# Performance work log

Hardware: AMD Instinct MI355X
Metric: run time of the kernel (lower is better)

The kernel has to match this reference:

```python
import jax, jax.numpy as jnp
import numpy as np

N = 100000   # nodes
E = 1600000  # edges (avg degree 16)
IN, HID, OUT = 128, 128, 64


def _glorot(key, shape):
    limit = np.sqrt(6.0 / (shape[0] + shape[1])).astype(np.float32)
    return jax.random.uniform(key, shape, jnp.float32, -limit, limit)


def setup_inputs() -> dict:
    key = jax.random.key(0)
    ks = jax.random.split(key, 12)
    inp = {}
    for i, (f, s, d) in enumerate([("feat1", "src1", "dst1"), ("feat2", "src2", "dst2"), ("feat", "src", "dst")]):
        inp[f] = jax.random.normal(ks[3 * i], (N, IN), jnp.float32)
        inp[s] = jax.random.randint(ks[3 * i + 1], (E,), 0, N, jnp.int32)
        inp[d] = jax.random.randint(ks[3 * i + 2], (E,), 0, N, jnp.int32)
    inp["W1"] = _glorot(ks[9], (IN, HID))
    inp["b1"] = jnp.zeros((HID,), jnp.float32)
    inp["W2"] = _glorot(ks[10], (HID, OUT))
    inp["b2"] = jnp.zeros((OUT,), jnp.float32)
    return inp


def _gcn_layer(x, src, dst, W, b):
    # DGL GraphConv norm='both': D_dst^{-1/2} * A * D_src^{-1/2} * X * W + b
    ones = jnp.ones(src.shape, jnp.float32)
    deg_out = jax.ops.segment_sum(ones, src, num_segments=N)
    deg_in = jax.ops.segment_sum(ones, dst, num_segments=N)
    norm_src = jax.lax.rsqrt(jnp.maximum(deg_out, 1.0))
    norm_dst = jax.lax.rsqrt(jnp.maximum(deg_in, 1.0))
    h = (x @ W) * norm_src[:, None]           # transform then normalize (math-equivalent order)
    agg = jax.ops.segment_sum(h[src], dst, num_segments=N)  # spmm aggregate
    return agg * norm_dst[:, None] + b


def _encoder(x, src, dst, W1, b1, W2, b2):
    h = jax.nn.relu(_gcn_layer(x, src, dst, W1, b1))
    return _gcn_layer(h, src, dst, W2, b2)


def reference(feat1, src1, dst1, feat2, src2, dst2, feat, src, dst, W1, b1, W2, b2):
    z1 = _encoder(feat1, src1, dst1, W1, b1, W2, b2)
    z2 = _encoder(feat2, src2, dst2, W1, b1, W2, b2)
    z = _encoder(feat, src, dst, W1, b1, W2, b2)
    return (z1, z2, z)
```

## Files before the change

### kernel.cpp

```cpp
#include <hip/hip_runtime.h>

#define NNODES 100000
#define NEDGES 1600000
#define FIN 128
#define FHID 128
#define FOUT 64

typedef unsigned short u16;
typedef unsigned char u8;
typedef unsigned int u32;
typedef __attribute__((ext_vector_type(8))) short short8;
typedef __attribute__((ext_vector_type(4))) float floatx4;

__device__ __forceinline__ u16 f2bf(float f) {
  u32 u = __float_as_uint(f);
  u32 r = (u + 0x7fffu + ((u >> 16) & 1u)) >> 16;
  return (u16)r;
}


#define NBUK 391
#define NSL2 250
#define SLICE2 (NEDGES / NSL2)

__global__ __launch_bounds__(256) void bucket_hist_kernel(const int* __restrict__ src,
                                                          const int* __restrict__ dst,
                                                          u32* __restrict__ part,
                                                          u32* __restrict__ part_src, int E) {
  __shared__ u32 hd[NBUK], hs[NBUK];
  const int s = blockIdx.x;
  for (int i = threadIdx.x; i < NBUK; i += 256) { hd[i] = 0; hs[i] = 0; }
  __syncthreads();
  const int e0 = s * SLICE2, e1 = min(e0 + SLICE2, E);
  const int i0 = e0 >> 2, i1 = e1 >> 2;
  for (int i = i0 + threadIdx.x; i < i1; i += 256) {
    int4 dv = ((const int4*)dst)[i];
    int4 sv = ((const int4*)src)[i];
    atomicAdd(&hd[(u32)dv.x >> 8], 1u);
    atomicAdd(&hd[(u32)dv.y >> 8], 1u);
    atomicAdd(&hd[(u32)dv.z >> 8], 1u);
    atomicAdd(&hd[(u32)dv.w >> 8], 1u);
    atomicAdd(&hs[(u32)sv.x >> 8], 1u);
    atomicAdd(&hs[(u32)sv.y >> 8], 1u);
    atomicAdd(&hs[(u32)sv.z >> 8], 1u);
    atomicAdd(&hs[(u32)sv.w >> 8], 1u);
  }
  __syncthreads();
  for (int i = threadIdx.x; i < NBUK; i += 256) {
    part[(size_t)s * NBUK + i] = hd[i];
    part_src[(size_t)s * NBUK + i] = hs[i];
  }
}

__global__ __launch_bounds__(512) void scan_part_kernel(u32* __restrict__ part_d,
                                                        u32* __restrict__ boff_d,
                                                        u32* __restrict__ bcount_d,
                                                        u32* __restrict__ part_s,
                                                        u32* __restrict__ boff_s,
                                                        u32* __restrict__ bcount_s) {
  u32* __restrict__ part = blockIdx.x ? part_s : part_d;
  u32* __restrict__ boff = blockIdx.x ? boff_s : boff_d;
  u32* __restrict__ bcount = blockIdx.x ? bcount_s : bcount_d;
  const int b = threadIdx.x;
  u32 run = 0;
  if (b < NBUK) {
#pragma unroll 5
    for (int s = 0; s < NSL2; s++) {
      u32 v = part[(size_t)s * NBUK + b];
      part[(size_t)s * NBUK + b] = run;
      run += v;
    }
  }
  __shared__ u32 sh[512];
  sh[threadIdx.x] = (b < NBUK) ? run : 0;
  __syncthreads();
  for (int d = 1; d < 512; d <<= 1) {
    u32 t = (threadIdx.x >= d) ? sh[threadIdx.x - d] : 0;
    __syncthreads();
    sh[threadIdx.x] += t;
    __syncthreads();
  }
  if (b < NBUK) {
    boff[b] = sh[threadIdx.x] - run;
    bcount[b] = run;
  }
}

__global__ __launch_bounds__(256) void scatter_kernel(const int* __restrict__ src,
                                                      const int* __restrict__ dst,
                                                      const u32* __restrict__ part,
                                                      const u32* __restrict__ boff,
                                                      const u32* __restrict__ part_src,
                                                      const u32* __restrict__ boff_src,
                                                      u32* __restrict__ pe,
                                                      u8* __restrict__ pes, int E) {
  __shared__ u32 cur[NBUK], curs[NBUK];
  const int s = blockIdx.x;
  for (int i = threadIdx.x; i < NBUK; i += 256) {
    cur[i] = part[(size_t)s * NBUK + i] + boff[i];
    curs[i] = part_src[(size_t)s * NBUK + i] + boff_src[i];
  }
  __syncthreads();
  const int e0 = s * SLICE2, e1 = min(e0 + SLICE2, E);
  const int i0 = e0 >> 2, i1 = e1 >> 2;
  for (int i = i0 + threadIdx.x; i < i1; i += 256) {
    int4 sv = ((const int4*)src)[i];
    int4 dv = ((const int4*)dst)[i];
    u32 p;
    p = atomicAdd(&cur[(u32)dv.x >> 8], 1u); pe[p] = ((u32)sv.x << 8) | ((u32)dv.x & 255u);
    p = atomicAdd(&cur[(u32)dv.y >> 8], 1u); pe[p] = ((u32)sv.y << 8) | ((u32)dv.y & 255u);
    p = atomicAdd(&cur[(u32)dv.z >> 8], 1u); pe[p] = ((u32)sv.z << 8) | ((u32)dv.z & 255u);
    p = atomicAdd(&cur[(u32)dv.w >> 8], 1u); pe[p] = ((u32)sv.w << 8) | ((u32)dv.w & 255u);
    p = atomicAdd(&curs[(u32)sv.x >> 8], 1u); pes[p] = (u8)((u32)sv.x & 255u);
    p = atomicAdd(&curs[(u32)sv.y >> 8], 1u); pes[p] = (u8)((u32)sv.y & 255u);
    p = atomicAdd(&curs[(u32)sv.z >> 8], 1u); pes[p] = (u8)((u32)sv.z & 255u);
    p = atomicAdd(&curs[(u32)sv.w >> 8], 1u); pes[p] = (u8)((u32)sv.w & 255u);
  }
}

__global__ __launch_bounds__(256) void bucket_csr_kernel(const u32* __restrict__ pe,
                                                         const u32* __restrict__ boff,
                                                         const u32* __restrict__ bcount,
                                                         int* __restrict__ csr,
                                                         int* __restrict__ offs,
                                                         int* __restrict__ deg_dst,
                                                         float* __restrict__ norm_dst, int n) {
  const int b = blockIdx.x;
  const int beg = (int)boff[b];
  const int cnt = (int)bcount[b];
  __shared__ int h[256], loc[256];
  const int t = threadIdx.x;
  h[t] = 0;
  __syncthreads();
  for (int i = t; i < cnt; i += 256) atomicAdd(&h[pe[beg + i] & 255u], 1);
  __syncthreads();
  const int myc = h[t];
  loc[t] = myc;
  __syncthreads();
  for (int d = 1; d < 256; d <<= 1) {
    int v = (t >= d) ? loc[t - d] : 0;
    __syncthreads();
    loc[t] += v;
    __syncthreads();
  }
  const int start = beg + loc[t] - myc;
  const int node = b * 256 + t;
  if (node < n) {
    offs[node] = start;
    deg_dst[node] = myc;
    norm_dst[node] = rsqrtf(fmaxf((float)myc, 1.0f));
  }
  __syncthreads();
  h[t] = start;
  __syncthreads();
  for (int i = t; i < cnt; i += 256) {
    u32 v = pe[beg + i];
    int p = atomicAdd(&h[v & 255u], 1);
    csr[p] = (int)(v >> 8);
  }
}

__global__ __launch_bounds__(256) void bucket_count_src_kernel(const u8* __restrict__ pes,
                                                               const u32* __restrict__ boff,
                                                               const u32* __restrict__ bcount,
                                                               float* __restrict__ norm_src,
                                                               int n) {
  const int b = blockIdx.x;
  const int beg = (int)boff[b];
  const int cnt = (int)bcount[b];
  __shared__ int h[256];
  h[threadIdx.x] = 0;
  __syncthreads();
  for (int i = threadIdx.x; i < cnt; i += 256) atomicAdd(&h[pes[beg + i]], 1);
  __syncthreads();
  const int node = b * 256 + threadIdx.x;
  if (node < n) norm_src[node] = rsqrtf(fmaxf((float)h[threadIdx.x], 1.0f));
}


#define XP 136

template <int CTOT, bool IN_BF16>
__global__ __launch_bounds__(256) void gemm_mfma(const void* __restrict__ Xv,
                                                 const float* __restrict__ W,
                                                 const float* __restrict__ norm,
                                                 u16* __restrict__ Y, int nrows) {
  __shared__ u16 Xs[64 * XP];
  __shared__ u16 Wt[64 * XP];
  __shared__ float norm_s[64];
  const int tid = threadIdx.x;
  const int row0 = blockIdx.x * 64;
  const int col0 = blockIdx.y * 64;

  if constexpr (IN_BF16) {
    const u16* X = (const u16*)Xv;
    for (int i = tid; i < 64 * 16; i += 256) {
      int r = i >> 4, k8 = (i & 15) * 8;
      int gr = row0 + r;
      uint4 v = make_uint4(0u, 0u, 0u, 0u);
      if (gr < nrows) v = *(const uint4*)&X[(size_t)gr * 128 + k8];
      *(uint4*)&Xs[r * XP + k8] = v;
    }
  } else {
    const float* X = (const float*)Xv;
    for (int i = tid; i < 64 * 32; i += 256) {
      int r = i >> 5, k4 = (i & 31) * 4;
      int gr = row0 + r;
      ushort4 o = make_ushort4(0, 0, 0, 0);
      if (gr < nrows) {
        float4 v = *(const float4*)&X[(size_t)gr * 128 + k4];
        o.x = f2bf(v.x); o.y = f2bf(v.y); o.z = f2bf(v.z); o.w = f2bf(v.w);
      }
      *(ushort4*)&Xs[r * XP + k4] = o;
    }
  }
  for (int i = tid; i < 128 * 16; i += 256) {
    int k = i >> 4, c4 = (i & 15) * 4;
    float4 v = *(const float4*)&W[(size_t)k * CTOT + col0 + c4];
    Wt[(c4 + 0) * XP + k] = f2bf(v.x);
    Wt[(c4 + 1) * XP + k] = f2bf(v.y);
    Wt[(c4 + 2) * XP + k] = f2bf(v.z);
    Wt[(c4 + 3) * XP + k] = f2bf(v.w);
  }
  if (tid < 64) norm_s[tid] = (row0 + tid < nrows) ? norm[row0 + tid] : 0.f;
  __syncthreads();

  const int w = tid >> 6, lane = tid & 63;
  const int quad = lane >> 4, r16 = lane & 15;
  const int arow = w * 16 + r16;

  short8 a[4];
#pragma unroll
  for (int kc = 0; kc < 4; kc++)
    a[kc] = *(const short8*)&Xs[arow * XP + kc * 32 + quad * 8];

#pragma unroll
  for (int nc = 0; nc < 4; nc++) {
    floatx4 acc = {0.f, 0.f, 0.f, 0.f};
#pragma unroll
    for (int kc = 0; kc < 4; kc++) {
      short8 b = *(const short8*)&Wt[(nc * 16 + r16) * XP + kc * 32 + quad * 8];
      acc = __builtin_amdgcn_mfma_f32_16x16x32_bf16(a[kc], b, acc, 0, 0, 0);
    }
#pragma unroll
    for (int i = 0; i < 4; i++) {
      int lr = w * 16 + quad * 4 + i;
      int gr = row0 + lr;
      if (gr < nrows)
        Y[(size_t)gr * CTOT + col0 + nc * 16 + r16] = f2bf(acc[i] * norm_s[lr]);
    }
  }
}


__device__ __forceinline__ void acc_row(float* acc, uint4 p) {
  acc[0] += __uint_as_float(p.x << 16);
  acc[1] += __uint_as_float(p.x & 0xffff0000u);
  acc[2] += __uint_as_float(p.y << 16);
  acc[3] += __uint_as_float(p.y & 0xffff0000u);
  acc[4] += __uint_as_float(p.z << 16);
  acc[5] += __uint_as_float(p.z & 0xffff0000u);
  acc[6] += __uint_as_float(p.w << 16);
  acc[7] += __uint_as_float(p.w & 0xffff0000u);
}

template <int F, bool RELU, bool OUT_BF16>
__global__ __launch_bounds__(256) void spmm_bf16(const u16* __restrict__ Hb,
                                                 const int* __restrict__ offs,
                                                 const int* __restrict__ deg,
                                                 const int* __restrict__ csr,
                                                 const float* __restrict__ norm_dst,
                                                 const float* __restrict__ bias,
                                                 void* __restrict__ Yv, int n) {
  constexpr int TPN = F / 8;
  constexpr int NPB = 256 / TPN;
  int node = blockIdx.x * NPB + threadIdx.x / TPN;
  if (node >= n) return;
  int f0 = (threadIdx.x % TPN) * 8;
  int beg = offs[node];
  int end = beg + deg[node];
  const u16* __restrict__ Hp = Hb + f0;
  float acc[8] = {};
  int e = beg;
  for (; e + 4 <= end; e += 4) {
    int s0 = csr[e + 0];
    int s1 = csr[e + 1];
    int s2 = csr[e + 2];
    int s3 = csr[e + 3];
    uint4 p0 = *(const uint4*)&Hp[(size_t)s0 * F];
    uint4 p1 = *(const uint4*)&Hp[(size_t)s1 * F];
    uint4 p2 = *(const uint4*)&Hp[(size_t)s2 * F];
    uint4 p3 = *(const uint4*)&Hp[(size_t)s3 * F];
    acc_row(acc, p0);
    acc_row(acc, p1);
    acc_row(acc, p2);
    acc_row(acc, p3);
  }
  for (; e < end; e++) {
    int s = csr[e];
    uint4 p = *(const uint4*)&Hp[(size_t)s * F];
    acc_row(acc, p);
  }
  float nd = norm_dst[node];
  float o[8];
#pragma unroll
  for (int i = 0; i < 8; i++) {
    o[i] = fmaf(acc[i], nd, bias[f0 + i]);
    if (RELU) o[i] = fmaxf(o[i], 0.f);
  }
  if constexpr (OUT_BF16) {
    u16* Y = (u16*)Yv;
    uint4 pk;
    pk.x = (u32)f2bf(o[0]) | ((u32)f2bf(o[1]) << 16);
    pk.y = (u32)f2bf(o[2]) | ((u32)f2bf(o[3]) << 16);
    pk.z = (u32)f2bf(o[4]) | ((u32)f2bf(o[5]) << 16);
    pk.w = (u32)f2bf(o[6]) | ((u32)f2bf(o[7]) << 16);
    *(uint4*)&Y[(size_t)node * F + f0] = pk;
  } else {
    float* Y = (float*)Yv;
    *(float4*)&Y[(size_t)node * F + f0] = make_float4(o[0], o[1], o[2], o[3]);
    *(float4*)&Y[(size_t)node * F + f0 + 4] = make_float4(o[4], o[5], o[6], o[7]);
  }
}


extern "C" void kernel_launch(void* const* d_in, const int* in_sizes, int n_in,
                              void* d_out, int out_size, void* d_ws, size_t ws_size,
                              hipStream_t stream) {
  const int N = NNODES;
  const int E = NEDGES;
  const float* W1 = (const float*)d_in[9];
  const float* b1 = (const float*)d_in[10];
  const float* W2 = (const float*)d_in[11];
  const float* b2 = (const float*)d_in[12];

  char* ws = (char*)d_ws;
  size_t off = 0;
  auto alloc = [&](size_t bytes) -> void* {
    void* p = ws + off;
    off += (bytes + 255) & ~(size_t)255;
    return p;
  };
  int* deg_dst = (int*)alloc((size_t)N * 4);
  float* norm_src = (float*)alloc((size_t)N * 4);
  float* norm_dst = (float*)alloc((size_t)N * 4);
  int* offs = (int*)alloc((size_t)N * 4);
  u32* boff = (u32*)alloc((size_t)NBUK * 4);
  u32* bcount = (u32*)alloc((size_t)NBUK * 4);
  u32* boff_s = (u32*)alloc((size_t)NBUK * 4);
  u32* bcount_s = (u32*)alloc((size_t)NBUK * 4);
  int* csr = (int*)alloc((size_t)E * 4);
  u16* H = (u16*)alloc((size_t)N * FHID * 2);
  u16* T = (u16*)alloc((size_t)N * FHID * 2);

  u32* part = (u32*)H;
  u32* part_src = part + (size_t)NSL2 * NBUK;
  u8* pes = (u8*)(part_src + (size_t)NSL2 * NBUK);
  u32* pe = (u32*)T;

  const int gemm_rb = (N + 63) / 64;

  for (int g = 0; g < 3; g++) {
    const float* feat = (const float*)d_in[3 * g + 0];
    const int* src = (const int*)d_in[3 * g + 1];
    const int* dst = (const int*)d_in[3 * g + 2];
    float* zout = (float*)d_out + (size_t)g * N * FOUT;

    bucket_hist_kernel<<<NSL2, 256, 0, stream>>>(src, dst, part, part_src, E);
    scan_part_kernel<<<2, 512, 0, stream>>>(part, boff, bcount, part_src, boff_s, bcount_s);
    scatter_kernel<<<NSL2, 256, 0, stream>>>(src, dst, part, boff, part_src, boff_s,
                                             pe, pes, E);
    bucket_csr_kernel<<<NBUK, 256, 0, stream>>>(pe, boff, bcount, csr, offs, deg_dst,
                                                norm_dst, N);
    bucket_count_src_kernel<<<NBUK, 256, 0, stream>>>(pes, boff_s, bcount_s, norm_src, N);

    gemm_mfma<FHID, false><<<dim3(gemm_rb, FHID / 64), 256, 0, stream>>>(
        feat, W1, norm_src, H, N);
    {
      constexpr int NPB = 256 / (FHID / 8);
      spmm_bf16<FHID, true, true><<<(N + NPB - 1) / NPB, 256, 0, stream>>>(
          H, offs, deg_dst, csr, norm_dst, b1, T, N);
    }

    gemm_mfma<FOUT, true><<<dim3(gemm_rb, FOUT / 64), 256, 0, stream>>>(
        T, W2, norm_src, H, N);
    {
      constexpr int NPB = 256 / (FOUT / 8);
      spmm_bf16<FOUT, false, false><<<(N + NPB - 1) / NPB, 256, 0, stream>>>(
          H, offs, deg_dst, csr, norm_dst, b2, zout, N);
    }
  }
}
```

Measured before the change: 829.3 us.

## Batch three graph encoders into single launches via grid z dimension

All nine per-graph kernels now take a blockIdx.z graph index and per-graph workspace slices, so the three encoders run as one launch per stage instead of three sequential launches. This targets launch overhead and low occupancy in the small kernels (scan, hist, csr) by filling the GPU with three graphs' work at once. It needs three times the workspace and falls back to the per-graph loop when the workspace is too small. The spmm gather loop is also software-pipelined so the next four rows load while the current four accumulate, at some extra register cost.

```diff
diff --git a/kernel.cpp b/kernel.cpp
--- a/kernel.cpp
+++ b/kernel.cpp
@@ -12,21 +12,32 @@
 typedef __attribute__((ext_vector_type(8))) short short8;
 typedef __attribute__((ext_vector_type(4))) float floatx4;
 
+#define NBUK 391
+#define NSL2 250
+#define SLICE2 (NEDGES / NSL2)
+#define SP ((size_t)NSL2 * NBUK)
+#define NH16 ((size_t)NNODES * FHID)
+
 __device__ __forceinline__ u16 f2bf(float f) {
   u32 u = __float_as_uint(f);
   u32 r = (u + 0x7fffu + ((u >> 16) & 1u)) >> 16;
   return (u16)r;
 }
 
-
-#define NBUK 391
-#define NSL2 250
-#define SLICE2 (NEDGES / NSL2)
-
-__global__ __launch_bounds__(256) void bucket_hist_kernel(const int* __restrict__ src,
-                                                          const int* __restrict__ dst,
-                                                          u32* __restrict__ part,
-                                                          u32* __restrict__ part_src, int E) {
+__device__ __forceinline__ const int* sel(const int* a, const int* b, const int* c, int z) {
+  return z == 0 ? a : (z == 1 ? b : c);
+}
+
+
+__global__ __launch_bounds__(256) void bucket_hist_kernel(
+    const int* s0, const int* s1, const int* s2,
+    const int* d0, const int* d1, const int* d2,
+    u16* __restrict__ Hbase, int E) {
+  const int z = blockIdx.z;
+  const int* __restrict__ src = sel(s0, s1, s2, z);
+  const int* __restrict__ dst = sel(d0, d1, d2, z);
+  u32* __restrict__ part = (u32*)(Hbase + (size_t)z * NH16);
+  u32* __restrict__ part_src = part + SP;
   __shared__ u32 hd[NBUK], hs[NBUK];
   const int s = blockIdx.x;
   for (int i = threadIdx.x; i < NBUK; i += 256) { hd[i] = 0; hs[i] = 0; }
@@ -52,15 +63,16 @@
   }
 }
 
-__global__ __launch_bounds__(512) void scan_part_kernel(u32* __restrict__ part_d,
+__global__ __launch_bounds__(512) void scan_part_kernel(u16* __restrict__ Hbase,
                                                         u32* __restrict__ boff_d,
                                                         u32* __restrict__ bcount_d,
-                                                        u32* __restrict__ part_s,
                                                         u32* __restrict__ boff_s,
                                                         u32* __restrict__ bcount_s) {
-  u32* __restrict__ part = blockIdx.x ? part_s : part_d;
-  u32* __restrict__ boff = blockIdx.x ? boff_s : boff_d;
-  u32* __restrict__ bcount = blockIdx.x ? bcount_s : bcount_d;
+  const int z = blockIdx.z;
+  u32* base = (u32*)(Hbase + (size_t)z * NH16);
+  u32* __restrict__ part = blockIdx.x ? base + SP : base;
+  u32* __restrict__ boff = (blockIdx.x ? boff_s : boff_d) + (size_t)z * NBUK;
+  u32* __restrict__ bcount = (blockIdx.x ? bcount_s : bcount_d) + (size_t)z * NBUK;
   const int b = threadIdx.x;
   u32 run = 0;
   if (b < NBUK) {
@@ -86,19 +98,25 @@
   }
 }
 
-__global__ __launch_bounds__(256) void scatter_kernel(const int* __restrict__ src,
-                                                      const int* __restrict__ dst,
-                                                      const u32* __restrict__ part,
-                                                      const u32* __restrict__ boff,
-                                                      const u32* __restrict__ part_src,
-                                                      const u32* __restrict__ boff_src,
-                                                      u32* __restrict__ pe,
-                                                      u8* __restrict__ pes, int E) {
+__global__ __launch_bounds__(256) void scatter_kernel(
+    const int* s0, const int* s1, const int* s2,
+    const int* d0, const int* d1, const int* d2,
+    u16* __restrict__ Hbase, u16* __restrict__ Tbase,
+    const u32* __restrict__ boff_d, const u32* __restrict__ boff_src, int E) {
+  const int z = blockIdx.z;
+  const int* __restrict__ src = sel(s0, s1, s2, z);
+  const int* __restrict__ dst = sel(d0, d1, d2, z);
+  const u32* __restrict__ part = (const u32*)(Hbase + (size_t)z * NH16);
+  const u32* __restrict__ part_src = part + SP;
+  u8* __restrict__ pes = (u8*)(part_src + SP);
+  u32* __restrict__ pe = (u32*)(Tbase + (size_t)z * NH16);
+  const u32* __restrict__ boff = boff_d + (size_t)z * NBUK;
+  const u32* __restrict__ boff_s = boff_src + (size_t)z * NBUK;
   __shared__ u32 cur[NBUK], curs[NBUK];
   const int s = blockIdx.x;
   for (int i = threadIdx.x; i < NBUK; i += 256) {
     cur[i] = part[(size_t)s * NBUK + i] + boff[i];
-    curs[i] = part_src[(size_t)s * NBUK + i] + boff_src[i];
+    curs[i] = part_src[(size_t)s * NBUK + i] + boff_s[i];
   }
   __syncthreads();
   const int e0 = s * SLICE2, e1 = min(e0 + SLICE2, E);
@@ -118,13 +136,21 @@
   }
 }
 
-__global__ __launch_bounds__(256) void bucket_csr_kernel(const u32* __restrict__ pe,
-                                                         const u32* __restrict__ boff,
-                                                         const u32* __restrict__ bcount,
-                                                         int* __restrict__ csr,
-                                                         int* __restrict__ offs,
-                                                         int* __restrict__ deg_dst,
-                                                         float* __restrict__ norm_dst, int n) {
+__global__ __launch_bounds__(256) void bucket_csr_kernel(const u16* __restrict__ Tbase,
+                                                         const u32* __restrict__ boffb,
+                                                         const u32* __restrict__ bcountb,
+                                                         int* __restrict__ csrb,
+                                                         int* __restrict__ offsb,
+                                                         int* __restrict__ degb,
+                                                         float* __restrict__ ndb, int n) {
+  const int z = blockIdx.z;
+  const u32* __restrict__ pe = (const u32*)(Tbase + (size_t)z * NH16);
+  int* __restrict__ csr = csrb + (size_t)z * NEDGES;
+  int* __restrict__ offs = offsb + (size_t)z * NNODES;
+  int* __restrict__ deg_dst = degb + (size_t)z * NNODES;
+  float* __restrict__ norm_dst = ndb + (size_t)z * NNODES;
+  const u32* boff = boffb + (size_t)z * NBUK;
+  const u32* bcount = bcountb + (size_t)z * NBUK;
   const int b = blockIdx.x;
   const int beg = (int)boff[b];
   const int cnt = (int)bcount[b];
@@ -160,11 +186,16 @@
   }
 }
 
-__global__ __launch_bounds__(256) void bucket_count_src_kernel(const u8* __restrict__ pes,
-                                                               const u32* __restrict__ boff,
-                                                               const u32* __restrict__ bcount,
-                                                               float* __restrict__ norm_src,
-                                                               int n) {
+__global__ __launch_bounds__(256) void bucket_count_src_kernel(const u16* __restrict__ Hbase,
+                                                               const u32* __restrict__ boffb,
+                                                               const u32* __restrict__ bcountb,
+                                                               float* __restrict__ nsb, int n) {
+  const int z = blockIdx.z;
+  const u32* partb = (const u32*)(Hbase + (size_t)z * NH16);
+  const u8* __restrict__ pes = (const u8*)(partb + 2 * SP);
+  const u32* boff = boffb + (size_t)z * NBUK;
+  const u32* bcount = bcountb + (size_t)z * NBUK;
+  float* __restrict__ norm_src = nsb + (size_t)z * NNODES;
   const int b = blockIdx.x;
   const int beg = (int)boff[b];
   const int cnt = (int)bcount[b];
@@ -181,10 +212,15 @@
 #define XP 136
 
 template <int CTOT, bool IN_BF16>
-__global__ __launch_bounds__(256) void gemm_mfma(const void* __restrict__ Xv,
+__global__ __launch_bounds__(256) void gemm_mfma(const void* X0, const void* X1,
+                                                 const void* X2,
                                                  const float* __restrict__ W,
-                                                 const float* __restrict__ norm,
-                                                 u16* __restrict__ Y, int nrows) {
+                                                 const float* __restrict__ normb,
+                                                 u16* __restrict__ Yb, int nrows) {
+  const int z = blockIdx.z;
+  const void* __restrict__ Xv = z == 0 ? X0 : (z == 1 ? X1 : X2);
+  const float* __restrict__ norm = normb + (size_t)z * NNODES;
+  u16* __restrict__ Y = Yb + (size_t)z * NNODES * CTOT;
   __shared__ u16 Xs[64 * XP];
   __shared__ u16 Wt[64 * XP];
   __shared__ float norm_s[64];
@@ -265,13 +301,19 @@
 }
 
 template <int F, bool RELU, bool OUT_BF16>
-__global__ __launch_bounds__(256) void spmm_bf16(const u16* __restrict__ Hb,
-                                                 const int* __restrict__ offs,
-                                                 const int* __restrict__ deg,
-                                                 const int* __restrict__ csr,
-                                                 const float* __restrict__ norm_dst,
+__global__ __launch_bounds__(256) void spmm_bf16(const u16* __restrict__ Hbase,
+                                                 const int* __restrict__ offsb,
+                                                 const int* __restrict__ degb,
+                                                 const int* __restrict__ csrb,
+                                                 const float* __restrict__ ndb,
                                                  const float* __restrict__ bias,
                                                  void* __restrict__ Yv, int n) {
+  const int z = blockIdx.z;
+  const u16* __restrict__ Hb = Hbase + (size_t)z * NNODES * F;
+  const int* __restrict__ offs = offsb + (size_t)z * NNODES;
+  const int* __restrict__ deg = degb + (size_t)z * NNODES;
+  const int* __restrict__ csr = csrb + (size_t)z * NEDGES;
+  const float* __restrict__ norm_dst = ndb + (size_t)z * NNODES;
   constexpr int TPN = F / 8;
   constexpr int NPB = 256 / TPN;
   int node = blockIdx.x * NPB + threadIdx.x / TPN;
@@ -282,19 +324,28 @@
   const u16* __restrict__ Hp = Hb + f0;
   float acc[8] = {};
   int e = beg;
-  for (; e + 4 <= end; e += 4) {
-    int s0 = csr[e + 0];
-    int s1 = csr[e + 1];
-    int s2 = csr[e + 2];
-    int s3 = csr[e + 3];
-    uint4 p0 = *(const uint4*)&Hp[(size_t)s0 * F];
-    uint4 p1 = *(const uint4*)&Hp[(size_t)s1 * F];
-    uint4 p2 = *(const uint4*)&Hp[(size_t)s2 * F];
-    uint4 p3 = *(const uint4*)&Hp[(size_t)s3 * F];
-    acc_row(acc, p0);
-    acc_row(acc, p1);
-    acc_row(acc, p2);
-    acc_row(acc, p3);
+  int nfull = (end - beg) >> 2;
+  if (nfull > 0) {
+    int sv[4]; uint4 p[4];
+#pragma unroll
+    for (int j = 0; j < 4; j++) sv[j] = csr[e + j];
+#pragma unroll
+    for (int j = 0; j < 4; j++) p[j] = *(const uint4*)&Hp[(size_t)sv[j] * F];
+    for (int b = 1; b < nfull; b++) {
+      e += 4;
+      int s2[4]; uint4 q[4];
+#pragma unroll
+      for (int j = 0; j < 4; j++) s2[j] = csr[e + j];
+#pragma unroll
+      for (int j = 0; j < 4; j++) q[j] = *(const uint4*)&Hp[(size_t)s2[j] * F];
+#pragma unroll
+      for (int j = 0; j < 4; j++) acc_row(acc, p[j]);
+#pragma unroll
+      for (int j = 0; j < 4; j++) p[j] = q[j];
+    }
+#pragma unroll
+    for (int j = 0; j < 4; j++) acc_row(acc, p[j]);
+    e += 4;
   }
   for (; e < end; e++) {
     int s = csr[e];
@@ -309,7 +360,7 @@
     if (RELU) o[i] = fmaxf(o[i], 0.f);
   }
   if constexpr (OUT_BF16) {
-    u16* Y = (u16*)Yv;
+    u16* Y = (u16*)Yv + (size_t)z * NNODES * F;
     uint4 pk;
     pk.x = (u32)f2bf(o[0]) | ((u32)f2bf(o[1]) << 16);
     pk.y = (u32)f2bf(o[2]) | ((u32)f2bf(o[3]) << 16);
@@ -317,7 +368,7 @@
     pk.w = (u32)f2bf(o[6]) | ((u32)f2bf(o[7]) << 16);
     *(uint4*)&Y[(size_t)node * F + f0] = pk;
   } else {
-    float* Y = (float*)Yv;
+    float* Y = (float*)Yv + (size_t)z * NNODES * F;
     *(float4*)&Y[(size_t)node * F + f0] = make_float4(o[0], o[1], o[2], o[3]);
     *(float4*)&Y[(size_t)node * F + f0 + 4] = make_float4(o[4], o[5], o[6], o[7]);
   }
@@ -334,6 +385,27 @@
   const float* W2 = (const float*)d_in[11];
   const float* b2 = (const float*)d_in[12];
 
+  const size_t HBYTES = NH16 * 2;
+
+  auto need_for = [&](size_t NG) -> size_t {
+    size_t o = 0;
+    auto al = [&](size_t b) { o = (o + b + 255) & ~(size_t)255; };
+    al(NG * N * 4);
+    al(NG * N * 4);
+    al(NG * N * 4);
+    al(NG * N * 4);
+    al(NG * NBUK * 4);
+    al(NG * NBUK * 4);
+    al(NG * NBUK * 4);
+    al(NG * NBUK * 4);
+    al(NG * (size_t)E * 4);
+    al(NG * HBYTES);
+    al(NG * HBYTES);
+    return o;
+  };
+  const bool batched = ws_size >= need_for(3);
+  const size_t NG = batched ? 3 : 1;
+
   char* ws = (char*)d_ws;
   size_t off = 0;
   auto alloc = [&](size_t bytes) -> void* {
@@ -341,53 +413,58 @@
     off += (bytes + 255) & ~(size_t)255;
     return p;
   };
-  int* deg_dst = (int*)alloc((size_t)N * 4);
-  float* norm_src = (float*)alloc((size_t)N * 4);
-  float* norm_dst = (float*)alloc((size_t)N * 4);
-  int* offs = (int*)alloc((size_t)N * 4);
-  u32* boff = (u32*)alloc((size_t)NBUK * 4);
-  u32* bcount = (u32*)alloc((size_t)NBUK * 4);
-  u32* boff_s = (u32*)alloc((size_t)NBUK * 4);
-  u32* bcount_s = (u32*)alloc((size_t)NBUK * 4);
-  int* csr = (int*)alloc((size_t)E * 4);
-  u16* H = (u16*)alloc((size_t)N * FHID * 2);
-  u16* T = (u16*)alloc((size_t)N * FHID * 2);
-
-  u32* part = (u32*)H;
-  u32* part_src = part + (size_t)NSL2 * NBUK;
-  u8* pes = (u8*)(part_src + (size_t)NSL2 * NBUK);
-  u32* pe = (u32*)T;
+  int* deg_dst = (int*)alloc(NG * N * 4);
+  float* norm_src = (float*)alloc(NG * N * 4);
+  float* norm_dst = (float*)alloc(NG * N * 4);
+  int* offs = (int*)alloc(NG * N * 4);
+  u32* boff = (u32*)alloc(NG * NBUK * 4);
+  u32* bcount = (u32*)alloc(NG * NBUK * 4);
+  u32* boff_s = (u32*)alloc(NG * NBUK * 4);
+  u32* bcount_s = (u32*)alloc(NG * NBUK * 4);
+  int* csr = (int*)alloc(NG * (size_t)E * 4);
+  u16* H = (u16*)alloc(NG * HBYTES);
+  u16* T = (u16*)alloc(NG * HBYTES);
 
   const int gemm_rb = (N + 63) / 64;
-
-  for (int g = 0; g < 3; g++) {
-    const float* feat = (const float*)d_in[3 * g + 0];
-    const int* src = (const int*)d_in[3 * g + 1];
-    const int* dst = (const int*)d_in[3 * g + 2];
-    float* zout = (float*)d_out + (size_t)g * N * FOUT;
-
-    bucket_hist_kernel<<<NSL2, 256, 0, stream>>>(src, dst, part, part_src, E);
-    scan_part_kernel<<<2, 512, 0, stream>>>(part, boff, bcount, part_src, boff_s, bcount_s);
-    scatter_kernel<<<NSL2, 256, 0, stream>>>(src, dst, part, boff, part_src, boff_s,
-                                             pe, pes, E);
-    bucket_csr_kernel<<<NBUK, 256, 0, stream>>>(pe, boff, bcount, csr, offs, deg_dst,
-                                                norm_dst, N);
-    bucket_count_src_kernel<<<NBUK, 256, 0, stream>>>(pes, boff_s, bcount_s, norm_src, N);
-
-    gemm_mfma<FHID, false><<<dim3(gemm_rb, FHID / 64), 256, 0, stream>>>(
-        feat, W1, norm_src, H, N);
-    {
-      constexpr int NPB = 256 / (FHID / 8);
-      spmm_bf16<FHID, true, true><<<(N + NPB - 1) / NPB, 256, 0, stream>>>(
-          H, offs, deg_dst, csr, norm_dst, b1, T, N);
-    }
-
-    gemm_mfma<FOUT, true><<<dim3(gemm_rb, FOUT / 64), 256, 0, stream>>>(
-        T, W2, norm_src, H, N);
-    {
-      constexpr int NPB = 256 / (FOUT / 8);
-      spmm_bf16<FOUT, false, false><<<(N + NPB - 1) / NPB, 256, 0, stream>>>(
-          H, offs, deg_dst, csr, norm_dst, b2, zout, N);
-    }
-  }
-}
+  const int nb1 = (N + 15) / 16;
+  const int nb2 = (N + 31) / 32;
+
+  auto run = [&](const int* s0, const int* s1, const int* s2,
+                 const int* d0, const int* d1, const int* d2,
+                 const float* f0, const float* f1, const float* f2,
+                 const void* x20, const void* x21, const void* x22,
+                 void* zoutv, unsigned gz) {
+    bucket_hist_kernel<<<dim3(NSL2, 1, gz), 256, 0, stream>>>(s0, s1, s2, d0, d1, d2, H, E);
+    scan_part_kernel<<<dim3(2, 1, gz), 512, 0, stream>>>(H, boff, bcount, boff_s, bcount_s);
+    scatter_kernel<<<dim3(NSL2, 1, gz), 256, 0, stream>>>(s0, s1, s2, d0, d1, d2,
+                                                          H, T, boff, boff_s, E);
+    bucket_csr_kernel<<<dim3(NBUK, 1, gz), 256, 0, stream>>>(T, boff, bcount, csr, offs,
+                                                             deg_dst, norm_dst, N);
+    bucket_count_src_kernel<<<dim3(NBUK, 1, gz), 256, 0, stream>>>(H, boff_s, bcount_s,
+                                                                   norm_src, N);
+    gemm_mfma<FHID, false><<<dim3(gemm_rb, FHID / 64, gz), 256, 0, stream>>>(
+        f0, f1, f2, W1, norm_src, H, N);
+    spmm_bf16<FHID, true, true><<<dim3(nb1, 1, gz), 256, 0, stream>>>(
+        H, offs, deg_dst, csr, norm_dst, b1, T, N);
+    gemm_mfma<FOUT, true><<<dim3(gemm_rb, FOUT / 64, gz), 256, 0, stream>>>(
+        x20, x21, x22, W2, norm_src, H, N);
+    spmm_bf16<FOUT, false, false><<<dim3(nb2, 1, gz), 256, 0, stream>>>(
+        H, offs, deg_dst, csr, norm_dst, b2, zoutv, N);
+  };
+
+  if (batched) {
+    run((const int*)d_in[1], (const int*)d_in[4], (const int*)d_in[7],
+        (const int*)d_in[2], (const int*)d_in[5], (const int*)d_in[8],
+        (const float*)d_in[0], (const float*)d_in[3], (const float*)d_in[6],
+        T, T + NH16, T + 2 * NH16,
+        d_out, 3);
+  } else {
+    for (int g = 0; g < 3; g++) {
+      const float* feat = (const float*)d_in[3 * g + 0];
+      const int* src = (const int*)d_in[3 * g + 1];
+      const int* dst = (const int*)d_in[3 * g + 2];
+      float* zout = (float*)d_out + (size_t)g * N * FOUT;
+      run(src, src, src, dst, dst, dst, feat, feat, feat, T, T, T, zout, 1);
+    }
+  }
+}
```

Measured after the change: 713.3 us. 1.16x faster.
